# Kernel tuning notes

Hardware: AMD Instinct MI355X
Metric: run time of the kernel (lower is better)

The kernel has to match this reference:

```python
import jax, jax.numpy as jnp
import numpy as np


def setup_inputs() -> dict:
    key = jax.random.key(0)
    k1, k2, k3 = jax.random.split(key, 3)
    B, N, D = 4, 256, 128
    s = jax.random.normal(k1, (B, N, D), dtype=jnp.float32)
    W1 = jax.random.normal(k2, (3 * D, 2 * D), dtype=jnp.float32) * 0.02
    b1 = jnp.zeros((2 * D,), dtype=jnp.float32)
    W2 = jax.random.normal(k3, (2 * D, 1), dtype=jnp.float32) * 0.02
    b2 = jnp.zeros((1,), dtype=jnp.float32)
    return {"s": s, "W1": W1, "b1": b1, "W2": W2, "b2": b2, "K": 8}


def reference(s, W1, b1, W2, b2, K):
    B, N, D = s.shape
    si = jnp.broadcast_to(s[:, :, None, :], (B, N, N, D))
    sj = jnp.broadcast_to(s[:, None, :, :], (B, N, N, D))
    pair = jnp.concatenate([si, sj, si * sj], axis=-1)  # [B,N,N,3D]
    h = jax.nn.relu(pair @ W1 + b1)                      # [B,N,N,2D]
    scores = (h @ W2 + b2)[..., 0]                       # [B,N,N]
    k = min(int(K), N)
    _, idx = jax.lax.top_k(scores, k)                    # [B,N,K]
    # scatter ones at topk indices (indices are distinct per row)
    gate = jnp.sum(jax.nn.one_hot(idx, N, dtype=jnp.float32), axis=-2)  # [B,N,N]
    w = gate / jnp.clip(jnp.sum(gate, axis=-1, keepdims=True), 1.0)
    ctx = jnp.einsum('bij,bjd->bid', w, s)               # [B,N,D]
    return ctx, gate, w
```

## Files before the change

kernel.cpp:

```cpp
#include <hip/hip_runtime.h>
#include <hip/hip_bf16.h>
#include <math.h>

#define B_ 4
#define N_ 256
#define D_ 128
#define H_ 256
#define K_ 8

typedef __attribute__((ext_vector_type(8))) short short8;
typedef __attribute__((ext_vector_type(4))) float f32x4;

__device__ __forceinline__ unsigned short f2bf(float x) {
    union { __hip_bfloat16 h; unsigned short s; } u;
    u.h = __float2bfloat16(x);
    return u.s;
}
__device__ __forceinline__ float bf2f(unsigned short b) {
    unsigned v = ((unsigned)b) << 16;
    return __builtin_bit_cast(float, v);
}
__device__ __forceinline__ unsigned pk2(float x, float y) {
    union { __hip_bfloat162 h; unsigned u; } c;
    c.h = __float22bfloat162_rn(float2{x, y});
    return c.u;
}
__device__ __forceinline__ void gld_lds16(const float* g, float* l) {
    __builtin_amdgcn_global_load_lds(
        (const __attribute__((address_space(1))) void*)g,
        (__attribute__((address_space(3))) void*)l, 16, 0, 0);
}

__global__ __launch_bounds__(256) void pre_kernel(
    const float* __restrict__ s, const float* __restrict__ W1,
    const float* __restrict__ b1,
    float* __restrict__ avec, float* __restrict__ bvec,
    unsigned short* __restrict__ Wt)
{
    int blk = blockIdx.x;
    int t = threadIdx.x;
    if (blk < 512) {
        int bi0 = blk * 2;
        __shared__ float s2[2][D_];
        {
            int r = t >> 7, d = t & 127;
            s2[r][d] = s[(size_t)(bi0 + r) * D_ + d];
        }
        __syncthreads();
        float aA0 = b1[t], aA1 = aA0, aB0 = 0.f, aB1 = 0.f;
        const float* W1a = W1 + t;
        const float* W1b = W1 + (size_t)D_ * H_ + t;
        #pragma unroll 8
        for (int d = 0; d < D_; ++d) {
            float wa = W1a[(size_t)d * H_];
            float wb = W1b[(size_t)d * H_];
            float s0 = s2[0][d], s1 = s2[1][d];
            aA0 = fmaf(s0, wa, aA0);
            aA1 = fmaf(s1, wa, aA1);
            aB0 = fmaf(s0, wb, aB0);
            aB1 = fmaf(s1, wb, aB1);
        }
        avec[(size_t)bi0 * H_ + t]       = aA0;
        avec[(size_t)(bi0 + 1) * H_ + t] = aA1;
        bvec[(size_t)bi0 * H_ + t]       = aB0;
        bvec[(size_t)(bi0 + 1) * H_ + t] = aB1;
    } else {
        int e = (blk - 512) * 256 + t;
        int h = e >> 7, d = e & 127;
        Wt[e] = f2bf(W1[(size_t)(2 * D_ + d) * H_ + h]);
    }
}

__global__ __launch_bounds__(512, 2) void approx_scores(
    const float* __restrict__ s, const unsigned short* __restrict__ Wt,
    const float* __restrict__ W2, const float* __restrict__ b2,
    const float* __restrict__ avec, const float* __restrict__ bvec,
    unsigned short* __restrict__ ascu)
{
    int blk = blockIdx.x;
    int b   = blk >> 7;
    int jtb = ((blk >> 4) & 7) * 32;
    int i0  = (blk & 15) * 16;
    int t = threadIdx.x;
    int lane = t & 63;
    int w = __builtin_amdgcn_readfirstlane(t >> 6);
    int l15 = lane & 15, quad = lane >> 4;

    __shared__ __align__(16) short Pl[2][32 * 128];
    __shared__ __align__(16) float si_all[16][D_];
    __shared__ __align__(16) float av_l[16][H_];
    __shared__ float partial[2][8][32];

    const float* sB = s + (size_t)b * N_ * D_;

    {
        const float* avp = avec + (size_t)(b * N_ + i0) * H_;
        #pragma unroll
        for (int k = 0; k < 2; ++k) {
            int slot = t + 512 * k;
            gld_lds16(avp + slot * 4, &av_l[0][0] + slot * 4);
        }
    }

    {
        int ii = t >> 5, dq = t & 31;
        *(float4*)&si_all[ii][dq * 4] =
            *(const float4*)(sB + (size_t)(i0 + ii) * D_ + dq * 4);
    }

    short8 Wreg[2][4];
    #pragma unroll
    for (int mi = 0; mi < 2; ++mi)
        #pragma unroll
        for (int dk = 0; dk < 4; ++dk)
            Wreg[mi][dk] = *(const short8*)(
                Wt + (size_t)(w * 32 + mi * 16 + l15) * D_ + dk * 32 + quad * 8);
    float bvr[2][2][4];
    float w2r[2][4];
    #pragma unroll
    for (int mi = 0; mi < 2; ++mi) {
        int hq = w * 32 + mi * 16 + quad * 4;
        #pragma unroll
        for (int r = 0; r < 4; ++r)
            w2r[mi][r] = W2[hq + r];
        #pragma unroll
        for (int nj = 0; nj < 2; ++nj)
            #pragma unroll
            for (int r = 0; r < 4; ++r)
                bvr[mi][nj][r] = bvec[((size_t)(b * N_ + jtb + nj * 16 + l15)) * H_
                                      + hq + r];
    }
    float b2v = b2[0];

    int prow = t >> 4, pseg = t & 15;
    float4 sj0, sj1;
    {
        const float* sj = sB + (size_t)(jtb + prow) * D_ + pseg * 8;
        sj0 = ((const float4*)sj)[0];
        sj1 = ((const float4*)sj)[1];
    }
    __syncthreads();

    {
        const float* si = &si_all[0][pseg * 8];
        float4 s0 = ((const float4*)si)[0], s1 = ((const float4*)si)[1];
        uint4 v;
        v.x = pk2(sj0.x * s0.x, sj0.y * s0.y);
        v.y = pk2(sj0.z * s0.z, sj0.w * s0.w);
        v.z = pk2(sj1.x * s1.x, sj1.y * s1.y);
        v.w = pk2(sj1.z * s1.z, sj1.w * s1.w);
        int pc = pseg ^ (prow & 15);
        *(uint4*)&Pl[0][prow * 128 + pc * 8] = v;
    }
    __syncthreads();

    #pragma unroll 1
    for (int i = 0; i < 16; ++i) {
        int cur = i & 1;
        if (w == 0 && lane < 32 && i > 0) {
            float sum = b2v;
            #pragma unroll
            for (int ww = 0; ww < 8; ++ww) sum += partial[(i - 1) & 1][ww][lane];
            ascu[(size_t)(b * N_ + i0 + i - 1) * N_ + jtb + lane] = f2bf(sum);
        }
        float4 av4[2];
        av4[0] = *(const float4*)&av_l[i][w * 32 + quad * 4];
        av4[1] = *(const float4*)&av_l[i][w * 32 + 16 + quad * 4];
        f32x4 acc[2][2];
        #pragma unroll
        for (int mi = 0; mi < 2; ++mi)
            #pragma unroll
            for (int nj = 0; nj < 2; ++nj)
                #pragma unroll
                for (int r = 0; r < 4; ++r)
                    acc[mi][nj][r] = av4[mi][r] + bvr[mi][nj][r];
        #pragma unroll
        for (int dk = 0; dk < 4; ++dk) {
            short8 Pf[2];
            #pragma unroll
            for (int nj = 0; nj < 2; ++nj) {
                int pcc = (dk * 4 + quad) ^ l15;
                Pf[nj] = *(const short8*)&Pl[cur][(nj * 16 + l15) * 128 + pcc * 8];
            }
            #pragma unroll
            for (int nj = 0; nj < 2; ++nj)
                #pragma unroll
                for (int mi = 0; mi < 2; ++mi)
                    acc[mi][nj] = __builtin_amdgcn_mfma_f32_16x16x32_bf16(
                        Wreg[mi][dk], Pf[nj], acc[mi][nj], 0, 0, 0);
        }
        if (i < 15) {
            const float* si = &si_all[i + 1][pseg * 8];
            float4 s0 = ((const float4*)si)[0], s1 = ((const float4*)si)[1];
            uint4 v;
            v.x = pk2(sj0.x * s0.x, sj0.y * s0.y);
            v.y = pk2(sj0.z * s0.z, sj0.w * s0.w);
            v.z = pk2(sj1.x * s1.x, sj1.y * s1.y);
            v.w = pk2(sj1.z * s1.z, sj1.w * s1.w);
            int pc = pseg ^ (prow & 15);
            *(uint4*)&Pl[cur ^ 1][prow * 128 + pc * 8] = v;
        }
        float rs[2];
        rs[0] = 0.f; rs[1] = 0.f;
        #pragma unroll
        for (int mi = 0; mi < 2; ++mi)
            #pragma unroll
            for (int nj = 0; nj < 2; ++nj)
                #pragma unroll
                for (int r = 0; r < 4; ++r)
                    rs[nj] = fmaf(fmaxf(acc[mi][nj][r], 0.f), w2r[mi][r], rs[nj]);
        #pragma unroll
        for (int nj = 0; nj < 2; ++nj) {
            rs[nj] += __shfl_xor(rs[nj], 16);
            rs[nj] += __shfl_xor(rs[nj], 32);
        }
        if (lane < 32) {
            float v = (quad == 0) ? rs[0] : rs[1];
            partial[cur][w][lane] = v;
        }
        __syncthreads();
    }
    if (w == 0 && lane < 32) {
        float sum = b2v;
        #pragma unroll
        for (int ww = 0; ww < 8; ++ww) sum += partial[15 & 1][ww][lane];
        ascu[(size_t)(b * N_ + i0 + 15) * N_ + jtb + lane] = f2bf(sum);
    }
}

#define DC8 8
__global__ __launch_bounds__(256) void finalize_kernel(
    const float* __restrict__ s, const float* __restrict__ W1,
    const float* __restrict__ W2, const float* __restrict__ b2,
    const float* __restrict__ avec, const float* __restrict__ bvec,
    const unsigned short* __restrict__ ascu,
    float* __restrict__ ctx, float* __restrict__ gate, float* __restrict__ w)
{
    int bi0 = blockIdx.x * 2;
    int b = bi0 >> 8;
    int t = threadIdx.x;

    __shared__ float asc[2][N_];
    __shared__ int cand[2][16];
    __shared__ __align__(16) float Pt[D_ * 32];
    __shared__ __align__(16) float Wl[2][DC8 * H_];
    __shared__ float part[2][16][33];
    __shared__ float rsc[2][16];
    __shared__ int sel8[2][8];

    for (int e = t; e < 512; e += 256) {
        int r = e >> 8, jj = e & 255;
        asc[r][jj] = bf2f(ascu[(size_t)(bi0 + r) * N_ + jj]);
    }
    __syncthreads();

    {
        int r = t >> 7, lj = t & 127;
        float my[2]; int rk[2];
        #pragma unroll
        for (int m = 0; m < 2; ++m) { my[m] = asc[r][m * 128 + lj]; rk[m] = 0; }
        #pragma unroll 4
        for (int j2 = 0; j2 < N_; ++j2) {
            float o = asc[r][j2];
            #pragma unroll
            for (int m = 0; m < 2; ++m) {
                int jm = m * 128 + lj;
                rk[m] += (o > my[m]) || (o == my[m] && j2 < jm);
            }
        }
        #pragma unroll
        for (int m = 0; m < 2; ++m)
            if (rk[m] < 16) cand[r][rk[m]] = m * 128 + lj;
    }
    __syncthreads();

    const float* Wc = W1 + (size_t)2 * D_ * H_;

    #pragma unroll
    for (int k = 0; k < 2; ++k) {
        int slot = t + 256 * k;
        gld_lds16(Wc + slot * 4, &Wl[0][slot * 4]);
    }

    for (int e = t; e < 1024; e += 256) {
        int rr = e >> 9, c = e & 15, dq = (e >> 4) & 31;
        int j = cand[rr][c];
        float4 sj = *(const float4*)(s + ((size_t)(b * N_ + j)) * D_ + dq * 4);
        float4 si = *(const float4*)(s + ((size_t)(bi0 + rr)) * D_ + dq * 4);
        int base = (dq * 4) * 32 + rr * 16 + c;
        Pt[base + 0 * 32] = si.x * sj.x;
        Pt[base + 1 * 32] = si.y * sj.y;
        Pt[base + 2 * 32] = si.z * sj.z;
        Pt[base + 3 * 32] = si.w * sj.w;
    }

    int cg = t & 3, rr = (t >> 2) & 1;
    int hg = t >> 3;
    int h0 = hg * 8;
    float acc[4][8];
    {
        const float* av = avec + (size_t)(bi0 + rr) * H_ + h0;
        float4 av40 = *(const float4*)(av);
        float4 av41 = *(const float4*)(av + 4);
        #pragma unroll
        for (int cc = 0; cc < 4; ++cc) {
            int j = cand[rr][cg * 4 + cc];
            const float* bv = bvec + ((size_t)(b * N_ + j)) * H_ + h0;
            float4 b40 = *(const float4*)(bv);
            float4 b41 = *(const float4*)(bv + 4);
            acc[cc][0] = av40.x + b40.x;
            acc[cc][1] = av40.y + b40.y;
            acc[cc][2] = av40.z + b40.z;
            acc[cc][3] = av40.w + b40.w;
            acc[cc][4] = av41.x + b41.x;
            acc[cc][5] = av41.y + b41.y;
            acc[cc][6] = av41.z + b41.z;
            acc[cc][7] = av41.w + b41.w;
        }
    }
    __syncthreads();

    int pvoff = rr * 16 + cg * 4;
    #pragma unroll 1
    for (int ch = 0; ch < 16; ++ch) {
        int cur = ch & 1;
        if (ch < 15) {
            const float* src = Wc + (size_t)(ch + 1) * DC8 * H_;
            #pragma unroll
            for (int k = 0; k < 2; ++k) {
                int slot = t + 256 * k;
                gld_lds16(src + slot * 4, &Wl[cur ^ 1][slot * 4]);
            }
        }
        int d0 = ch * DC8;
        #pragma unroll
        for (int d = 0; d < DC8; ++d) {
            float4 pv = *(const float4*)&Pt[(d0 + d) * 32 + pvoff];
            float wv[8];
            *(float4*)&wv[0] = *(const float4*)&Wl[cur][d * H_ + h0];
            *(float4*)&wv[4] = *(const float4*)&Wl[cur][d * H_ + h0 + 4];
            #pragma unroll
            for (int m = 0; m < 8; ++m) {
                acc[0][m] = fmaf(pv.x, wv[m], acc[0][m]);
                acc[1][m] = fmaf(pv.y, wv[m], acc[1][m]);
                acc[2][m] = fmaf(pv.z, wv[m], acc[2][m]);
                acc[3][m] = fmaf(pv.w, wv[m], acc[3][m]);
            }
        }
        __syncthreads();
    }

    {
        float w2v[8];
        *(float4*)&w2v[0] = *(const float4*)(W2 + h0);
        *(float4*)&w2v[4] = *(const float4*)(W2 + h0 + 4);
        #pragma unroll
        for (int cc = 0; cc < 4; ++cc) {
            float sc = 0.f;
            #pragma unroll
            for (int m = 0; m < 8; ++m)
                sc = fmaf(fmaxf(acc[cc][m], 0.f), w2v[m], sc);
            part[rr][cg * 4 + cc][hg] = sc;
        }
    }
    __syncthreads();
    if (t < 32) {
        int r2 = t >> 4, c2 = t & 15;
        float sum = b2[0];
        #pragma unroll
        for (int m = 0; m < 32; ++m) sum += part[r2][c2][m];
        rsc[r2][c2] = sum;
    }
    __syncthreads();

    if (t < 32) {
        int r2 = t >> 4, c2 = t & 15;
        float my = rsc[r2][c2]; int myj = cand[r2][c2];
        int rank = 0;
        #pragma unroll
        for (int c3 = 0; c3 < 16; ++c3) {
            float o = rsc[r2][c3]; int oj = cand[r2][c3];
            rank += (o > my) || (o == my && oj < myj);
        }
        if (rank < 8) sel8[r2][rank] = myj;
    }
    __syncthreads();

    for (int e = t; e < 512; e += 256) {
        int r2 = e >> 8, jj = e & 255;
        float gv = 0.f;
        #pragma unroll
        for (int m = 0; m < 8; ++m)
            gv = (jj == sel8[r2][m]) ? 1.f : gv;
        gate[(size_t)(bi0 + r2) * N_ + jj] = gv;
        w[(size_t)(bi0 + r2) * N_ + jj]    = gv * 0.125f;
    }
    {
        int r2 = t >> 7, d = t & 127;
        float a = 0.f;
        #pragma unroll
        for (int m = 0; m < 8; ++m)
            a += s[((size_t)(b * N_ + sel8[r2][m])) * D_ + d];
        ctx[(size_t)(bi0 + r2) * D_ + d] = a * 0.125f;
    }
}

extern "C" void kernel_launch(void* const* d_in, const int* in_sizes, int n_in,
                              void* d_out, int out_size, void* d_ws, size_t ws_size,
                              hipStream_t stream)
{
    const float* s  = (const float*)d_in[0];
    const float* W1 = (const float*)d_in[1];
    const float* b1 = (const float*)d_in[2];
    const float* W2 = (const float*)d_in[3];
    const float* b2 = (const float*)d_in[4];

    float* avec = (float*)d_ws;
    float* bvec = avec + (size_t)B_ * N_ * H_;
    unsigned short* ascu = (unsigned short*)(bvec + (size_t)B_ * N_ * H_);
    unsigned short* Wtu  = ascu + (size_t)B_ * N_ * N_;

    float* ctx  = (float*)d_out;
    float* gate = ctx + (size_t)B_ * N_ * D_;
    float* wout = gate + (size_t)B_ * N_ * N_;

    pre_kernel<<<640, 256, 0, stream>>>(s, W1, b1, avec, bvec, Wtu);
    approx_scores<<<512, 512, 0, stream>>>(s, Wtu, W2, b2, avec, bvec, ascu);
    finalize_kernel<<<B_ * N_ / 2, 256, 0, stream>>>(s, W1, W2, b2, avec, bvec, ascu,
                                                     ctx, gate, wout);
}
```

Baseline: 130.1 us.

## Partition W1 staging per wavefront to drop block barriers in finalize loop

Splits the shared W1 chunk buffer so each wavefront loads and consumes only its own 64-column slice. Each wave can then wait on its own async global-to-LDS loads with s_waitcnt vmcnt instead of a block-wide __syncthreads per chunk, and the last chunk is peeled out of the loop. This removes 16 block barriers per block. It relies on each wave writing exactly the data it reads and on the vmcnt counts matching the outstanding loads, which is fragile if the compiler reorders other memory ops.

```diff
diff --git a/kernel.cpp b/kernel.cpp
--- a/kernel.cpp
+++ b/kernel.cpp
@@ -239,11 +239,13 @@
     int bi0 = blockIdx.x * 2;
     int b = bi0 >> 8;
     int t = threadIdx.x;
+    int lane = t & 63;
+    int wv_id = t >> 6;
 
     __shared__ float asc[2][N_];
     __shared__ int cand[2][16];
     __shared__ __align__(16) float Pt[D_ * 32];
-    __shared__ __align__(16) float Wl[2][DC8 * H_];
+    __shared__ __align__(16) float Wlw[4][2][DC8][64];
     __shared__ float part[2][16][33];
     __shared__ float rsc[2][16];
     __shared__ int sel8[2][8];
@@ -276,11 +278,13 @@
 
     const float* Wc = W1 + (size_t)2 * D_ * H_;
 
+    int dl = lane >> 4;
+    int hl = (lane & 15) * 4;
+
     #pragma unroll
-    for (int k = 0; k < 2; ++k) {
-        int slot = t + 256 * k;
-        gld_lds16(Wc + slot * 4, &Wl[0][slot * 4]);
-    }
+    for (int k = 0; k < 2; ++k)
+        gld_lds16(Wc + (size_t)(k * 4 + dl) * H_ + wv_id * 64 + hl,
+                  &Wlw[wv_id][0][k * 4 + dl][hl]);
 
     for (int e = t; e < 1024; e += 256) {
         int rr = e >> 9, c = e & 15, dq = (e >> 4) & 31;
@@ -297,6 +301,7 @@
     int cg = t & 3, rr = (t >> 2) & 1;
     int hg = t >> 3;
     int h0 = hg * 8;
+    int ho = (hg & 7) * 8;
     float acc[4][8];
     {
         const float* av = avec + (size_t)(bi0 + rr) * H_ + h0;
@@ -322,32 +327,51 @@
 
     int pvoff = rr * 16 + cg * 4;
     #pragma unroll 1
-    for (int ch = 0; ch < 16; ++ch) {
+    for (int ch = 0; ch < 15; ++ch) {
         int cur = ch & 1;
-        if (ch < 15) {
-            const float* src = Wc + (size_t)(ch + 1) * DC8 * H_;
-            #pragma unroll
-            for (int k = 0; k < 2; ++k) {
-                int slot = t + 256 * k;
-                gld_lds16(src + slot * 4, &Wl[cur ^ 1][slot * 4]);
-            }
-        }
+        {
+            const float* src = Wc + (size_t)((ch + 1) * DC8) * H_;
+            #pragma unroll
+            for (int k = 0; k < 2; ++k)
+                gld_lds16(src + (size_t)(k * 4 + dl) * H_ + wv_id * 64 + hl,
+                          &Wlw[wv_id][cur ^ 1][k * 4 + dl][hl]);
+        }
+        asm volatile("s_waitcnt vmcnt(2)" ::: "memory");
+        __builtin_amdgcn_sched_barrier(0);
         int d0 = ch * DC8;
         #pragma unroll
         for (int d = 0; d < DC8; ++d) {
             float4 pv = *(const float4*)&Pt[(d0 + d) * 32 + pvoff];
-            float wv[8];
-            *(float4*)&wv[0] = *(const float4*)&Wl[cur][d * H_ + h0];
-            *(float4*)&wv[4] = *(const float4*)&Wl[cur][d * H_ + h0 + 4];
+            float wvv[8];
+            *(float4*)&wvv[0] = *(const float4*)&Wlw[wv_id][cur][d][ho];
+            *(float4*)&wvv[4] = *(const float4*)&Wlw[wv_id][cur][d][ho + 4];
             #pragma unroll
             for (int m = 0; m < 8; ++m) {
-                acc[0][m] = fmaf(pv.x, wv[m], acc[0][m]);
-                acc[1][m] = fmaf(pv.y, wv[m], acc[1][m]);
-                acc[2][m] = fmaf(pv.z, wv[m], acc[2][m]);
-                acc[3][m] = fmaf(pv.w, wv[m], acc[3][m]);
+                acc[0][m] = fmaf(pv.x, wvv[m], acc[0][m]);
+                acc[1][m] = fmaf(pv.y, wvv[m], acc[1][m]);
+                acc[2][m] = fmaf(pv.z, wvv[m], acc[2][m]);
+                acc[3][m] = fmaf(pv.w, wvv[m], acc[3][m]);
             }
         }
-        __syncthreads();
+    }
+    asm volatile("s_waitcnt vmcnt(0)" ::: "memory");
+    __builtin_amdgcn_sched_barrier(0);
+    {
+        int d0 = 15 * DC8;
+        #pragma unroll
+        for (int d = 0; d < DC8; ++d) {
+            float4 pv = *(const float4*)&Pt[(d0 + d) * 32 + pvoff];
+            float wvv[8];
+            *(float4*)&wvv[0] = *(const float4*)&Wlw[wv_id][1][d][ho];
+            *(float4*)&wvv[4] = *(const float4*)&Wlw[wv_id][1][d][ho + 4];
+            #pragma unroll
+            for (int m = 0; m < 8; ++m) {
+                acc[0][m] = fmaf(pv.x, wvv[m], acc[0][m]);
+                acc[1][m] = fmaf(pv.y, wvv[m], acc[1][m]);
+                acc[2][m] = fmaf(pv.z, wvv[m], acc[2][m]);
+                acc[3][m] = fmaf(pv.w, wvv[m], acc[3][m]);
+            }
+        }
     }
 
     {
```

After: 128.6 us. No clear change (-1.2%).
